# Kernel tuning notes

Measured on AMD Instinct MI355X. Metric: run time of the kernel, lower is better.

Reference implementation:

```python
import jax, jax.numpy as jnp
import numpy as np
from jax import lax

NPOINTS = [1024, 256, 64, 16]
RADII = [0.02, 0.04, 0.06, 0.08]
NSAMPLE = [32, 32, 16, 16]
# per-level MLP widths; first entry already includes the +3 for use_xyz concat
MLPS = [[6, 32, 32, 64], [67, 64, 64, 128], [131, 128, 128, 256], [259, 256, 256, 512]]
EPS = 1e-5


def setup_inputs() -> dict:
    key = jax.random.key(0)
    B, N = 8, 16384
    pc = jax.random.uniform(jax.random.fold_in(key, 0), (B, N, 6), jnp.float32)
    # xyz into a 0.2-cube so the hard-coded radii (0.02..0.08) find real neighborhoods
    pc = pc.at[..., :3].multiply(0.2)
    inp = {"pointcloud": pc}
    ki = 1
    for l, m in enumerate(MLPS):
        for j in range(len(m) - 1):
            cin, cout = m[j], m[j + 1]
            inp[f"w{l}{j}"] = jax.random.normal(jax.random.fold_in(key, ki), (cin, cout), jnp.float32) * (1.0 / float(np.sqrt(cin)))
            inp[f"g{l}{j}"] = jnp.ones((cout,), jnp.float32)
            inp[f"b{l}{j}"] = jnp.zeros((cout,), jnp.float32)
            ki += 1
    return inp


def _fps(xyz, npoint):
    # iterative farthest point sampling, start at index 0 (matches CUDA kernel)
    B, N, _ = xyz.shape

    def step(carry, _):
        mind, last = carry
        lastp = jnp.take_along_axis(xyz, last[:, None, None], axis=1)  # [B,1,3]
        d = jnp.sum((xyz - lastp) ** 2, axis=-1)                       # [B,N]
        mind = jnp.minimum(mind, d)
        nxt = jnp.argmax(mind, axis=1).astype(jnp.int32)
        return (mind, nxt), last

    init = (jnp.full((B, N), 1e10, xyz.dtype), jnp.zeros((B,), jnp.int32))
    _, idx = lax.scan(step, init, None, length=npoint)
    return jnp.transpose(idx)  # [B,npoint]


def _gather(pts, idx):
    # pts [B,N,C], idx [B,...] -> [B,...,C]
    return jax.vmap(lambda p, i: p[i])(pts, idx)


def _ball_query(xyz, centers, radius, nsample):
    # first nsample points (in index order) within radius; pad with first hit (0 if none)
    N = xyz.shape[1]
    d2 = jnp.sum((centers[:, :, None, :] - xyz[:, None, :, :]) ** 2, axis=-1)  # [B,S,N]
    key = jnp.where(d2 < radius * radius, jnp.arange(N, dtype=jnp.int32), N)
    negtop, _ = lax.top_k(-key, nsample)
    sel = -negtop                      # ascending candidate indices
    valid = sel < N
    first = jnp.where(valid[..., :1], sel[..., :1], 0)
    return jnp.where(valid, sel, first)  # [B,S,nsample] int32


def _sa(xyz, feats, npoint, radius, nsample, layers):
    fps_idx = lax.stop_gradient(_fps(xyz, npoint))
    new_xyz = _gather(xyz, fps_idx)                    # [B,S,3]
    idx = _ball_query(xyz, new_xyz, radius, nsample)   # [B,S,K]
    g = _gather(xyz, idx) - new_xyz[:, :, None, :]     # centered grouped xyz [B,S,K,3]
    g = jnp.concatenate([g, _gather(feats, idx)], axis=-1)  # use_xyz concat -> [B,S,K,3+C]
    x = g
    for W, gamma, beta in layers:
        x = jnp.einsum('bski,io->bsko', x, W)          # 1x1 conv, bias=False (bn on)
        mu = jnp.mean(x, axis=(0, 1, 2))               # BN training-mode batch stats
        var = jnp.var(x, axis=(0, 1, 2))
        x = jax.nn.relu(gamma * (x - mu) * lax.rsqrt(var + EPS) + beta)
    return new_xyz, jnp.max(x, axis=2)                 # max-pool over neighbors -> [B,S,Cout]


def reference(pointcloud, w00, g00, b00, w01, g01, b01, w02, g02, b02,
              w10, g10, b10, w11, g11, b11, w12, g12, b12,
              w20, g20, b20, w21, g21, b21, w22, g22, b22,
              w30, g30, b30, w31, g31, b31, w32, g32, b32):
    params = [
        [(w00, g00, b00), (w01, g01, b01), (w02, g02, b02)],
        [(w10, g10, b10), (w11, g11, b11), (w12, g12, b12)],
        [(w20, g20, b20), (w21, g21, b21), (w22, g22, b22)],
        [(w30, g30, b30), (w31, g31, b31), (w32, g32, b32)],
    ]
    xyz = pointcloud[..., :3]
    feats = pointcloud[..., 3:]   # channels-last (torch keeps [B,C,N]; pure layout diff)
    l_xyz, l_feats = [xyz], [feats]
    for k in range(4):
        nx, nf = _sa(l_xyz[k], l_feats[k], NPOINTS[k], RADII[k], NSAMPLE[k], params[k])
        l_xyz.append(nx)
        l_feats.append(nf)
    return tuple(l_xyz) + tuple(l_feats)
```

## Files before the change

kernel.cpp:

```cpp
#include <hip/hip_runtime.h>

#define WAVE 64

__global__ __launch_bounds__(256) void split_kernel(const float* __restrict__ pc,
    float* __restrict__ xyz, float* __restrict__ feats, int total) {
  int t = blockIdx.x * blockDim.x + threadIdx.x;
  if (t >= total) return;
  const float* p = pc + (size_t)t * 6;
  xyz[t * 3 + 0] = p[0]; xyz[t * 3 + 1] = p[1]; xyz[t * 3 + 2] = p[2];
  feats[t * 3 + 0] = p[3]; feats[t * 3 + 1] = p[4]; feats[t * 3 + 2] = p[5];
}

__global__ __launch_bounds__(256) void zero_kernel(float* __restrict__ p, int n) {
  int t = blockIdx.x * blockDim.x + threadIdx.x;
  if (t < n) p[t] = 0.f;
}

__device__ __forceinline__ unsigned long long dpp_max_u64(unsigned long long v) {
#define DPP_STEP_U64(ctrl) { \
    unsigned lo_ = (unsigned)v, hi_ = (unsigned)(v >> 32); \
    unsigned tlo_ = (unsigned)__builtin_amdgcn_update_dpp((int)lo_, (int)lo_, ctrl, 0xf, 0xf, false); \
    unsigned thi_ = (unsigned)__builtin_amdgcn_update_dpp((int)hi_, (int)hi_, ctrl, 0xf, 0xf, false); \
    unsigned long long t_ = ((unsigned long long)thi_ << 32) | tlo_; \
    if (t_ > v) v = t_; }
  DPP_STEP_U64(0x111) DPP_STEP_U64(0x112) DPP_STEP_U64(0x114)
  DPP_STEP_U64(0x118) DPP_STEP_U64(0x142) DPP_STEP_U64(0x143)
#undef DPP_STEP_U64
  return v;
}

#define FPS_W   8
#define FPS_PT  8
__global__ __launch_bounds__(256, 4) void fps_big_multi_kernel(
    const float* __restrict__ xyz, float* __restrict__ new_xyz,
    unsigned long long* __restrict__ gkey, int N, int S) {
  const int b = blockIdx.x & 7;
  const int w = blockIdx.x >> 3;
  const int tid = threadIdx.x;
  const int lane = tid & 63;
  const int wv = tid >> 6;
  const float* px = xyz + (size_t)b * N * 3;
  const int base = w * (FPS_PT * 256);
  __shared__ unsigned long long s_cand[4];
  __shared__ unsigned long long s_win;
  float rx[FPS_PT], ry[FPS_PT], rz[FPS_PT], mind[FPS_PT];
#pragma unroll
  for (int p = 0; p < FPS_PT; ++p) {
    int i = base + p * 256 + tid;
    rx[p] = px[i * 3 + 0]; ry[p] = px[i * 3 + 1]; rz[p] = px[i * 3 + 2];
    asm volatile("" : "+v"(rx[p]), "+v"(ry[p]), "+v"(rz[p]));
    mind[p] = 1e10f;
  }
  float qx = px[0], qy = px[1], qz = px[2];
  if (w == 0 && tid == 0) {
    float* o = new_xyz + (size_t)b * S * 3;
    o[0] = qx; o[1] = qy; o[2] = qz;
  }
  unsigned long long* slots = gkey + (size_t)b * S * FPS_W;
  for (unsigned it = 1; it < (unsigned)S; ++it) {
    float bestv = -1.f; unsigned besti = 0;
#pragma unroll
    for (int p = 0; p < FPS_PT; ++p) {
      float dx = __fsub_rn(rx[p], qx);
      float dy = __fsub_rn(ry[p], qy);
      float dz = __fsub_rn(rz[p], qz);
      float d = __fadd_rn(__fadd_rn(__fmul_rn(dx, dx), __fmul_rn(dy, dy)), __fmul_rn(dz, dz));
      float mo = fminf(mind[p], d);
      mind[p] = mo;
      if (mo > bestv) { bestv = mo; besti = (unsigned)(base + p * 256 + tid); }
    }
    unsigned long long key = ((unsigned long long)__float_as_uint(bestv) << 32)
                           | (0xFFFFFFFFu - besti);
    key = dpp_max_u64(key);
    if (lane == 63) s_cand[wv] = key;
    __syncthreads();
    if (tid < 64) {
      unsigned long long k = s_cand[lane & 3];
#pragma unroll
      for (int off = 1; off < 4; off <<= 1) {
        unsigned long long o = __shfl_xor(k, off, 4);
        if (o > k) k = o;
      }
      if (lane == 0) {
        atomicExch(&slots[(size_t)it * FPS_W + w], k);
      }
      unsigned long long kk = 0ull;
      if (lane < FPS_W) {
        unsigned long long* sl = &slots[(size_t)it * FPS_W + lane];
        unsigned long long t0 = __builtin_amdgcn_s_memrealtime();
        int r = 0;
        for (;;) {
          kk = __hip_atomic_load(sl, __ATOMIC_RELAXED, __HIP_MEMORY_SCOPE_AGENT);
          if (kk) break;
          if (++r > 256) {
            kk = atomicMax(sl, 0ull);
            if (kk) break;
            if (__builtin_amdgcn_s_memrealtime() - t0 > 2000000ull) {
              kk = 0xFFFFFFFFull;
              break;
            }
            __builtin_amdgcn_s_sleep(1);
          }
        }
      }
#pragma unroll
      for (int off = 1; off < FPS_W; off <<= 1) {
        unsigned long long o = __shfl_xor(kk, off, FPS_W);
        if (o > kk) kk = o;
      }
      if (lane == 0) s_win = kk;
    }
    __syncthreads();
    unsigned long long k = s_win;
    int last = (int)((0xFFFFFFFFu - (unsigned)k) & 16383u);
    const float* q = px + (size_t)last * 3;
    qx = q[0]; qy = q[1]; qz = q[2];
    if (w == 0 && tid == 0) {
      float* o = new_xyz + ((size_t)b * S + it) * 3;
      o[0] = qx; o[1] = qy; o[2] = qz;
    }
  }
}

__global__ void fps_small_kernel(const float* __restrict__ xyz,
    float* __restrict__ new_xyz, int N, int S) {
  const int b = blockIdx.x;
  const int tid = threadIdx.x;
  const int lane = tid & 63;
  const int wv = tid >> 6;
  const int NW = N >> 6;
  const float* px = xyz + (size_t)b * N * 3;
  __shared__ float sx[1024], sy[1024], sz[1024];
  __shared__ unsigned long long s_cand[2][16];
  float x = px[tid * 3 + 0], y = px[tid * 3 + 1], z = px[tid * 3 + 2];
  sx[tid] = x; sy[tid] = y; sz[tid] = z;
  float mind = 1e10f;
  float qx = px[0], qy = px[1], qz = px[2];
  if (tid == 0) {
    float* o = new_xyz + (size_t)b * S * 3;
    o[0] = qx; o[1] = qy; o[2] = qz;
  }
  __syncthreads();
  for (unsigned it = 1; it < (unsigned)S; ++it) {
    float dx = __fsub_rn(x, qx);
    float dy = __fsub_rn(y, qy);
    float dz = __fsub_rn(z, qz);
    float d = __fadd_rn(__fadd_rn(__fmul_rn(dx, dx), __fmul_rn(dy, dy)), __fmul_rn(dz, dz));
    mind = fminf(mind, d);
    unsigned long long key = ((unsigned long long)__float_as_uint(mind) << 32)
                           | (0xFFFFFFFFu - (unsigned)tid);
    key = dpp_max_u64(key);
    if (lane == 63) s_cand[it & 1u][wv] = key;
    __syncthreads();
    unsigned long long k = (lane < NW) ? s_cand[it & 1u][lane] : 0ull;
    k = dpp_max_u64(k);
    unsigned klo = (unsigned)__builtin_amdgcn_readlane((int)(unsigned)k, 63);
    int last = (int)(0xFFFFFFFFu - klo);
    qx = sx[last]; qy = sy[last]; qz = sz[last];
    if (tid == 0) {
      float* o = new_xyz + ((size_t)b * S + it) * 3;
      o[0] = qx; o[1] = qy; o[2] = qz;
    }
  }
}

__global__ __launch_bounds__(256) void ballquery_kernel(const float* __restrict__ xyz,
    const float* __restrict__ centers, int* __restrict__ out_idx,
    int N, int S, int nsample, float r2) {
  int gw = (blockIdx.x * blockDim.x + threadIdx.x) >> 6;
  int lane = threadIdx.x & 63;
  int b = gw / S;
  int s = gw - b * S;
  const float* px = xyz + (size_t)b * N * 3;
  const float* cp = centers + ((size_t)b * S + s) * 3;
  float cx = cp[0], cy = cp[1], cz = cp[2];
  int* out = out_idx + ((size_t)b * S + s) * nsample;
  int cnt = 0;
  int firsti = 0;
  for (int base = 0; base < N; base += WAVE) {
    int i = base + lane;
    float dx = __fsub_rn(cx, px[i * 3 + 0]);
    float dy = __fsub_rn(cy, px[i * 3 + 1]);
    float dz = __fsub_rn(cz, px[i * 3 + 2]);
    float d = __fadd_rn(__fadd_rn(__fmul_rn(dx, dx), __fmul_rn(dy, dy)), __fmul_rn(dz, dz));
    bool hit = d < r2;
    unsigned long long m = __ballot(hit);
    if (hit) {
      int slot = cnt + __popcll(m & ((1ull << lane) - 1ull));
      if (slot < nsample) out[slot] = i;
    }
    if (cnt == 0 && m) firsti = base + __ffsll((unsigned long long)m) - 1;
    cnt += __popcll(m);
    if (cnt >= nsample) break;
  }
  for (int q = cnt + lane; q < nsample; q += WAVE) out[q] = firsti;
}

__global__ __launch_bounds__(256) void group_kernel(const float* __restrict__ xyz,
    const float* __restrict__ feats, const float* __restrict__ centers,
    const int* __restrict__ idx, float* __restrict__ X,
    int N, int S, int K, int ci, int R) {
  int t = blockIdx.x * blockDim.x + threadIdx.x;
  int C0 = ci + 3;
  int r = t / C0;
  if (r >= R) return;
  int c = t - r * C0;
  int g = r / K;
  int b = g / S;
  int j = idx[r];
  float v;
  if (c < 3) v = __fsub_rn(xyz[((size_t)b * N + j) * 3 + c], centers[(size_t)g * 3 + c]);
  else       v = feats[((size_t)b * N + j) * ci + (c - 3)];
  X[(size_t)r * C0 + c] = v;
}

#define BM 64
#define BN 64
#define BK 16
__global__ __launch_bounds__(256) void mm_fused_kernel(const float* __restrict__ A,
    const float* __restrict__ W, float* __restrict__ Y,
    float* __restrict__ st_out, const float* __restrict__ st_in,
    const float* __restrict__ g_in, const float* __restrict__ b_in,
    int R, int C, int Co, float inv_n) {
  __shared__ float As[BK][BM + 4];
  __shared__ float Bs[BK][BN + 4];
  __shared__ float s_mu[260], s_rs[260], s_g[260], s_b[260];
  __shared__ float s_sum[BN], s_sq[BN];
  int r0 = blockIdx.x * BM;
  int n0 = blockIdx.y * BN;
  int tid = threadIdx.x;
  int tx = tid & 15, ty = tid >> 4;
  if (st_in) {
    for (int c = tid; c < C; c += 256) {
      float mu = st_in[c] * inv_n;
      float var = st_in[512 + c] * inv_n - mu * mu;
      s_mu[c] = mu; s_rs[c] = rsqrtf(var + 1e-5f);
      s_g[c] = g_in[c]; s_b[c] = b_in[c];
    }
  }
  if (tid < BN) { s_sum[tid] = 0.f; s_sq[tid] = 0.f; }
  __syncthreads();
  float acc[4][4] = {};
  for (int k0 = 0; k0 < C; k0 += BK) {
#pragma unroll
    for (int u = 0; u < 4; ++u) {
      int lin = tid + u * 256;
      int row = lin >> 4;
      int cc = lin & 15;
      int c = k0 + cc;
      float v = 0.f;
      if (c < C) {
        v = A[(size_t)(r0 + row) * C + c];
        if (st_in) {
          v = s_g[c] * ((v - s_mu[c]) * s_rs[c]) + s_b[c];
          v = v > 0.f ? v : 0.f;
        }
      }
      As[cc][row] = v;
    }
#pragma unroll
    for (int u = 0; u < 4; ++u) {
      int lin = tid + u * 256;
      int kk = lin >> 6;
      int n = lin & 63;
      int c = k0 + kk;
      Bs[kk][n] = (c < C && (n0 + n) < Co) ? W[(size_t)c * Co + n0 + n] : 0.f;
    }
    __syncthreads();
#pragma unroll
    for (int kk = 0; kk < BK; ++kk) {
      float a0[4], b0[4];
#pragma unroll
      for (int i = 0; i < 4; ++i) a0[i] = As[kk][ty * 4 + i];
#pragma unroll
      for (int jj = 0; jj < 4; ++jj) b0[jj] = Bs[kk][tx * 4 + jj];
#pragma unroll
      for (int i = 0; i < 4; ++i)
#pragma unroll
        for (int jj = 0; jj < 4; ++jj)
          acc[i][jj] = fmaf(a0[i], b0[jj], acc[i][jj]);
    }
    __syncthreads();
  }
#pragma unroll
  for (int i = 0; i < 4; ++i) {
    int r = r0 + ty * 4 + i;
#pragma unroll
    for (int jj = 0; jj < 4; ++jj) {
      int n = n0 + tx * 4 + jj;
      if (n < Co) Y[(size_t)r * Co + n] = acc[i][jj];
    }
  }
#pragma unroll
  for (int jj = 0; jj < 4; ++jj) {
    float cs = 0.f, cq = 0.f;
#pragma unroll
    for (int i = 0; i < 4; ++i) { float v = acc[i][jj]; cs += v; cq += v * v; }
    atomicAdd(&s_sum[tx * 4 + jj], cs);
    atomicAdd(&s_sq[tx * 4 + jj], cq);
  }
  __syncthreads();
  if (tid < BN) {
    int n = n0 + tid;
    if (n < Co) {
      atomicAdd(&st_out[n], s_sum[tid]);
      atomicAdd(&st_out[512 + n], s_sq[tid]);
    }
  }
}

__global__ __launch_bounds__(256) void norm_relu_max_kernel(const float* __restrict__ Y,
    float* __restrict__ O, const float* __restrict__ st,
    const float* __restrict__ gamma, const float* __restrict__ beta,
    int G, int K, int Co, float inv_n) {
  int t = blockIdx.x * blockDim.x + threadIdx.x;
  if (t >= G * Co) return;
  int c = t & (Co - 1);
  int g = t / Co;
  float mu = st[c] * inv_n;
  float var = st[512 + c] * inv_n - mu * mu;
  float rs = rsqrtf(var + 1e-5f);
  float ga = gamma[c], be = beta[c];
  const float* yp = Y + (size_t)g * K * Co + c;
  float m = -1e30f;
  for (int k = 0; k < K; ++k) {
    float v = ga * ((yp[(size_t)k * Co] - mu) * rs) + be;
    m = fmaxf(m, v);
  }
  O[t] = m > 0.f ? m : 0.f;
}

extern "C" void kernel_launch(void* const* d_in, const int* in_sizes, int n_in,
                              void* d_out, int out_size, void* d_ws, size_t ws_size,
                              hipStream_t stream) {
  const float* pc = (const float*)d_in[0];
  float* out = (float*)d_out;
  char* wsb = (char*)d_ws;

  int* ballidx = (int*)wsb;
  float* stats = (float*)(wsb + ((size_t)1 << 20));
  unsigned long long* gkey = (unsigned long long*)(wsb + ((size_t)2 << 20));
  float* bufA = (float*)(wsb + ((size_t)3 << 20));
  float* bufB = (float*)(wsb + ((size_t)37 << 20));

  const int B = 8;
  static const int Ns[4] = {16384, 1024, 256, 64};
  static const int Ss[4] = {1024, 256, 64, 16};
  static const int Ks[4] = {32, 32, 16, 16};
  static const double Rr[4] = {0.02, 0.04, 0.06, 0.08};
  static const int Ci[4] = {3, 64, 128, 256};
  static const int mlp[4][4] = {{6,32,32,64},{67,64,64,128},{131,128,128,256},{259,256,256,512}};
  static const size_t ox[5] = {0, 393216, 417792, 423936, 425472};
  static const size_t of[5] = {425856, 819072, 1343360, 1605504, 1736576};

  split_kernel<<<(B * 16384 + 255) / 256, 256, 0, stream>>>(pc, out + ox[0], out + of[0], B * 16384);
  zero_kernel<<<(524288 + 255) / 256, 256, 0, stream>>>(stats, 524288);

  for (int l = 0; l < 4; ++l) {
    const float* xyz = out + ox[l];
    const float* fts = out + of[l];
    float* nxyz = out + ox[l + 1];
    const int N = Ns[l], S = Ss[l], K = Ks[l], ci = Ci[l], C0 = ci + 3;
    const float r2 = (float)(Rr[l] * Rr[l]);

    if (l == 0) fps_big_multi_kernel<<<B * FPS_W, 256, 0, stream>>>(xyz, nxyz, gkey, N, S);
    else        fps_small_kernel<<<B, N, 0, stream>>>(xyz, nxyz, N, S);

    ballquery_kernel<<<(B * S) / 4, 256, 0, stream>>>(xyz, nxyz, ballidx, N, S, K, r2);

    const int R = B * S * K;
    {
      int total = R * C0;
      group_kernel<<<(total + 255) / 256, 256, 0, stream>>>(xyz, fts, nxyz, ballidx, bufA,
                                                            N, S, K, ci, R);
    }

    const float inv_n = 1.0f / (float)R;
    float* X = bufA; float* Y = bufB;
    const float* prev_st = nullptr;
    const float* prev_g = nullptr;
    const float* prev_b = nullptr;
    for (int j = 0; j < 3; ++j) {
      const int cin = mlp[l][j], cout = mlp[l][j + 1];
      const float* Wt = (const float*)d_in[1 + (l * 3 + j) * 3 + 0];
      const float* Ga = (const float*)d_in[1 + (l * 3 + j) * 3 + 1];
      const float* Be = (const float*)d_in[1 + (l * 3 + j) * 3 + 2];
      float* st = stats + (size_t)(l * 3 + j) * 1024;
      dim3 grid(R / 64, (cout + 63) / 64);
      mm_fused_kernel<<<grid, 256, 0, stream>>>(X, Wt, Y, st, prev_st, prev_g, prev_b,
                                                R, cin, cout, inv_n);
      if (j < 2) {
        prev_st = st; prev_g = Ga; prev_b = Be;
        float* tswap = X; X = Y; Y = tswap;
      } else {
        int G = B * S;
        int tot = G * cout;
        norm_relu_max_kernel<<<(tot + 255) / 256, 256, 0, stream>>>(Y, out + of[l + 1], st, Ga, Be,
                                                                    G, K, cout, inv_n);
      }
    }
  }
}
```

Before: 2.415 ms.

## Fuse grouping gather into first GEMM and max-pool into last GEMM epilogue

The first MLP matmul now gathers grouped neighbor coordinates and features straight from the ball-query indices, so the separate group kernel and its intermediate buffer go away. The last matmul no longer writes its full output. It keeps per-group channel max and min in order-preserving unsigned form in shared memory and writes only those. A small final kernel applies batch norm using whichever extreme matches gamma's sign, then ReLU. This cuts global traffic for the largest intermediates and removes launches, at the cost of irregular gather loads inside the GEMM tile loop and extra shared-memory atomics.

Measured after the change: 2.388 ms. Within noise of the previous version (-1.1%).

```diff
diff --git a/kernel.cpp b/kernel.cpp
--- a/kernel.cpp
+++ b/kernel.cpp
@@ -14,6 +14,15 @@
 __global__ __launch_bounds__(256) void zero_kernel(float* __restrict__ p, int n) {
   int t = blockIdx.x * blockDim.x + threadIdx.x;
   if (t < n) p[t] = 0.f;
+}
+
+__device__ __forceinline__ unsigned mapf(float f) {
+  unsigned b = __float_as_uint(f);
+  return (b & 0x80000000u) ? ~b : (b | 0x80000000u);
+}
+__device__ __forceinline__ float unmapf(unsigned u) {
+  unsigned b = (u & 0x80000000u) ? (u ^ 0x80000000u) : ~u;
+  return __uint_as_float(b);
 }
 
 __device__ __forceinline__ unsigned long long dpp_max_u64(unsigned long long v) {
@@ -196,24 +205,6 @@
   for (int q = cnt + lane; q < nsample; q += WAVE) out[q] = firsti;
 }
 
-__global__ __launch_bounds__(256) void group_kernel(const float* __restrict__ xyz,
-    const float* __restrict__ feats, const float* __restrict__ centers,
-    const int* __restrict__ idx, float* __restrict__ X,
-    int N, int S, int K, int ci, int R) {
-  int t = blockIdx.x * blockDim.x + threadIdx.x;
-  int C0 = ci + 3;
-  int r = t / C0;
-  if (r >= R) return;
-  int c = t - r * C0;
-  int g = r / K;
-  int b = g / S;
-  int j = idx[r];
-  float v;
-  if (c < 3) v = __fsub_rn(xyz[((size_t)b * N + j) * 3 + c], centers[(size_t)g * 3 + c]);
-  else       v = feats[((size_t)b * N + j) * ci + (c - 3)];
-  X[(size_t)r * C0 + c] = v;
-}
-
 #define BM 64
 #define BN 64
 #define BK 16
@@ -221,11 +212,17 @@
     const float* __restrict__ W, float* __restrict__ Y,
     float* __restrict__ st_out, const float* __restrict__ st_in,
     const float* __restrict__ g_in, const float* __restrict__ b_in,
-    int R, int C, int Co, float inv_n) {
+    int R, int C, int Co, float inv_n,
+    const int* __restrict__ idx, const float* __restrict__ xyz,
+    const float* __restrict__ feats, const float* __restrict__ centers,
+    int N, int kshift, int sshift, int ci,
+    unsigned* __restrict__ extmax, unsigned* __restrict__ extmin) {
   __shared__ float As[BK][BM + 4];
   __shared__ float Bs[BK][BN + 4];
   __shared__ float s_mu[260], s_rs[260], s_g[260], s_b[260];
   __shared__ float s_sum[BN], s_sq[BN];
+  __shared__ int s_idx[BM];
+  __shared__ unsigned s_mx[4][BN], s_mn[4][BN];
   int r0 = blockIdx.x * BM;
   int n0 = blockIdx.y * BN;
   int tid = threadIdx.x;
@@ -238,7 +235,14 @@
       s_g[c] = g_in[c]; s_b[c] = b_in[c];
     }
   }
+  if (idx && tid < BM) s_idx[tid] = idx[r0 + tid];
   if (tid < BN) { s_sum[tid] = 0.f; s_sq[tid] = 0.f; }
+  if (extmax) {
+    for (int t2 = tid; t2 < 4 * BN; t2 += 256) {
+      ((unsigned*)s_mx)[t2] = 0u;
+      ((unsigned*)s_mn)[t2] = 0xFFFFFFFFu;
+    }
+  }
   __syncthreads();
   float acc[4][4] = {};
   for (int k0 = 0; k0 < C; k0 += BK) {
@@ -250,10 +254,20 @@
       int c = k0 + cc;
       float v = 0.f;
       if (c < C) {
-        v = A[(size_t)(r0 + row) * C + c];
-        if (st_in) {
-          v = s_g[c] * ((v - s_mu[c]) * s_rs[c]) + s_b[c];
-          v = v > 0.f ? v : 0.f;
+        if (idx) {
+          int r = r0 + row;
+          int g = r >> kshift;
+          int bb = g >> sshift;
+          int j = s_idx[row];
+          if (c < 3) v = __fsub_rn(xyz[((size_t)bb * N + j) * 3 + c],
+                                   centers[(size_t)g * 3 + c]);
+          else       v = feats[((size_t)bb * N + j) * ci + (c - 3)];
+        } else {
+          v = A[(size_t)(r0 + row) * C + c];
+          if (st_in) {
+            v = s_g[c] * ((v - s_mu[c]) * s_rs[c]) + s_b[c];
+            v = v > 0.f ? v : 0.f;
+          }
         }
       }
       As[cc][row] = v;
@@ -282,13 +296,27 @@
     }
     __syncthreads();
   }
-#pragma unroll
-  for (int i = 0; i < 4; ++i) {
-    int r = r0 + ty * 4 + i;
+  if (!extmax) {
+#pragma unroll
+    for (int i = 0; i < 4; ++i) {
+      int r = r0 + ty * 4 + i;
+#pragma unroll
+      for (int jj = 0; jj < 4; ++jj) {
+        int n = n0 + tx * 4 + jj;
+        if (n < Co) Y[(size_t)r * Co + n] = acc[i][jj];
+      }
+    }
+  } else {
+    int gi = (ty * 4) >> kshift;
 #pragma unroll
     for (int jj = 0; jj < 4; ++jj) {
-      int n = n0 + tx * 4 + jj;
-      if (n < Co) Y[(size_t)r * Co + n] = acc[i][jj];
+      float mx = acc[0][jj], mn = acc[0][jj];
+#pragma unroll
+      for (int i = 1; i < 4; ++i) {
+        mx = fmaxf(mx, acc[i][jj]); mn = fminf(mn, acc[i][jj]);
+      }
+      atomicMax(&s_mx[gi][tx * 4 + jj], mapf(mx));
+      atomicMin(&s_mn[gi][tx * 4 + jj], mapf(mn));
     }
   }
 #pragma unroll
@@ -307,27 +335,35 @@
       atomicAdd(&st_out[512 + n], s_sq[tid]);
     }
   }
-}
-
-__global__ __launch_bounds__(256) void norm_relu_max_kernel(const float* __restrict__ Y,
+  if (extmax) {
+    int gpb = BM >> kshift;
+    if (tid < gpb * BN) {
+      int gi = tid >> 6;
+      int n = tid & 63;
+      if (n0 + n < Co) {
+        size_t o = (size_t)((r0 >> kshift) + gi) * Co + n0 + n;
+        extmax[o] = s_mx[gi][n];
+        extmin[o] = s_mn[gi][n];
+      }
+    }
+  }
+}
+
+__global__ __launch_bounds__(256) void norm_max_final_kernel(
+    const unsigned* __restrict__ extmax, const unsigned* __restrict__ extmin,
     float* __restrict__ O, const float* __restrict__ st,
     const float* __restrict__ gamma, const float* __restrict__ beta,
-    int G, int K, int Co, float inv_n) {
+    int total, int Co, float inv_n) {
   int t = blockIdx.x * blockDim.x + threadIdx.x;
-  if (t >= G * Co) return;
+  if (t >= total) return;
   int c = t & (Co - 1);
-  int g = t / Co;
   float mu = st[c] * inv_n;
   float var = st[512 + c] * inv_n - mu * mu;
   float rs = rsqrtf(var + 1e-5f);
   float ga = gamma[c], be = beta[c];
-  const float* yp = Y + (size_t)g * K * Co + c;
-  float m = -1e30f;
-  for (int k = 0; k < K; ++k) {
-    float v = ga * ((yp[(size_t)k * Co] - mu) * rs) + be;
-    m = fmaxf(m, v);
-  }
-  O[t] = m > 0.f ? m : 0.f;
+  float y = (ga >= 0.f) ? unmapf(extmax[t]) : unmapf(extmin[t]);
+  float v = ga * ((y - mu) * rs) + be;
+  O[t] = v > 0.f ? v : 0.f;
 }
 
 extern "C" void kernel_launch(void* const* d_in, const int* in_sizes, int n_in,
@@ -340,13 +376,17 @@
   int* ballidx = (int*)wsb;
   float* stats = (float*)(wsb + ((size_t)1 << 20));
   unsigned long long* gkey = (unsigned long long*)(wsb + ((size_t)2 << 20));
-  float* bufA = (float*)(wsb + ((size_t)3 << 20));
-  float* bufB = (float*)(wsb + ((size_t)37 << 20));
+  unsigned* extmax = (unsigned*)(wsb + ((size_t)3 << 20));
+  unsigned* extmin = (unsigned*)(wsb + ((size_t)5 << 20));
+  float* bufA = (float*)(wsb + ((size_t)8 << 20));
+  float* bufB = (float*)(wsb + ((size_t)42 << 20));
 
   const int B = 8;
   static const int Ns[4] = {16384, 1024, 256, 64};
   static const int Ss[4] = {1024, 256, 64, 16};
   static const int Ks[4] = {32, 32, 16, 16};
+  static const int Ksh[4] = {5, 5, 4, 4};
+  static const int Ssh[4] = {10, 8, 6, 4};
   static const double Rr[4] = {0.02, 0.04, 0.06, 0.08};
   static const int Ci[4] = {3, 64, 128, 256};
   static const int mlp[4][4] = {{6,32,32,64},{67,64,64,128},{131,128,128,256},{259,256,256,512}};
@@ -360,21 +400,16 @@
     const float* xyz = out + ox[l];
     const float* fts = out + of[l];
     float* nxyz = out + ox[l + 1];
-    const int N = Ns[l], S = Ss[l], K = Ks[l], ci = Ci[l], C0 = ci + 3;
+    const int N = Ns[l], S = Ss[l], K = Ks[l], ci = Ci[l];
     const float r2 = (float)(Rr[l] * Rr[l]);
+    (void)K;
 
     if (l == 0) fps_big_multi_kernel<<<B * FPS_W, 256, 0, stream>>>(xyz, nxyz, gkey, N, S);
     else        fps_small_kernel<<<B, N, 0, stream>>>(xyz, nxyz, N, S);
 
-    ballquery_kernel<<<(B * S) / 4, 256, 0, stream>>>(xyz, nxyz, ballidx, N, S, K, r2);
-
-    const int R = B * S * K;
-    {
-      int total = R * C0;
-      group_kernel<<<(total + 255) / 256, 256, 0, stream>>>(xyz, fts, nxyz, ballidx, bufA,
-                                                            N, S, K, ci, R);
-    }
-
+    ballquery_kernel<<<(B * S) / 4, 256, 0, stream>>>(xyz, nxyz, ballidx, N, S, Ks[l], r2);
+
+    const int R = B * S * Ks[l];
     const float inv_n = 1.0f / (float)R;
     float* X = bufA; float* Y = bufB;
     const float* prev_st = nullptr;
@@ -386,18 +421,23 @@
       const float* Ga = (const float*)d_in[1 + (l * 3 + j) * 3 + 1];
       const float* Be = (const float*)d_in[1 + (l * 3 + j) * 3 + 2];
       float* st = stats + (size_t)(l * 3 + j) * 1024;
+      const bool last = (j == 2);
       dim3 grid(R / 64, (cout + 63) / 64);
-      mm_fused_kernel<<<grid, 256, 0, stream>>>(X, Wt, Y, st, prev_st, prev_g, prev_b,
-                                                R, cin, cout, inv_n);
-      if (j < 2) {
+      mm_fused_kernel<<<grid, 256, 0, stream>>>(
+          (j == 0) ? nullptr : X, Wt, last ? nullptr : Y, st,
+          prev_st, prev_g, prev_b, R, cin, cout, inv_n,
+          (j == 0) ? ballidx : nullptr, xyz, fts, nxyz,
+          N, Ksh[l], Ssh[l], ci,
+          last ? extmax : nullptr, last ? extmin : nullptr);
+      if (!last) {
         prev_st = st; prev_g = Ga; prev_b = Be;
         float* tswap = X; X = Y; Y = tswap;
       } else {
         int G = B * S;
         int tot = G * cout;
-        norm_relu_max_kernel<<<(tot + 255) / 256, 256, 0, stream>>>(Y, out + of[l + 1], st, Ga, Be,
-                                                                    G, K, cout, inv_n);
-      }
-    }
-  }
-}
+        norm_max_final_kernel<<<(tot + 255) / 256, 256, 0, stream>>>(
+            extmax, extmin, out + of[l + 1], st, Ga, Be, tot, cout, inv_n);
+      }
+    }
+  }
+}
```
